# Kernel tuning notes

Hardware: AMD Instinct MI355X
Metric: run time of the kernel (lower is better)

## Reference

```python
import jax, jax.numpy as jnp
import numpy as np

THR = 0.001
EPS = 1e-5
GROUPS = 32

def ternary_weight(w):
    wc = jnp.clip(w, -1.0, 1.0)
    return jnp.where(wc > THR, 1.0, jnp.where(wc < -THR, -1.0, 0.0))

def fake_quant(x, scale):
    s = jnp.abs(scale)
    return jnp.clip(jnp.round(x / s), -1.0, 1.0) * s

def group_norm(x, gamma, beta):
    b, c, h, w = x.shape
    xg = x.reshape(b, GROUPS, c // GROUPS, h, w)
    mu = xg.mean(axis=(2, 3, 4), keepdims=True)
    var = xg.var(axis=(2, 3, 4), keepdims=True)
    xn = (xg - mu) * jax.lax.rsqrt(var + EPS)
    return xn.reshape(b, c, h, w) * gamma[None, :, None, None] + beta[None, :, None, None]

def conv2d(x, w, b, pad):
    out = jax.lax.conv_general_dilated(x, w, (1, 1), [(pad, pad), (pad, pad)],
                                       dimension_numbers=('NCHW', 'OIHW', 'NCHW'))
    return out + b[None, :, None, None]

def setup_inputs() -> dict:
    key = jax.random.key(0)
    ks = jax.random.split(key, 10)
    B, Cin, Cout, H, W, T = 8, 256, 256, 64, 64, 512
    return {
        'x': jax.random.normal(ks[0], (B, Cin, H, W), jnp.float32),
        'time_emb': jax.random.normal(ks[1], (B, T), jnp.float32),
        'gn1_g': jnp.ones((Cin,), jnp.float32),
        'gn1_b': jnp.zeros((Cin,), jnp.float32),
        'scale1': jnp.array(1.0, jnp.float32),
        'W1': jax.random.normal(ks[2], (Cout, Cin, 3, 3), jnp.float32) * 0.05,
        'b1': jax.random.normal(ks[3], (Cout,), jnp.float32) * 0.01,
        'Wt': jax.random.normal(ks[4], (Cout, T), jnp.float32) * 0.05,
        'bt': jax.random.normal(ks[5], (Cout,), jnp.float32) * 0.01,
        'gn2_g': jnp.ones((Cout,), jnp.float32),
        'gn2_b': jnp.zeros((Cout,), jnp.float32),
        'scale2': jnp.array(1.0, jnp.float32),
        'W2': jax.random.normal(ks[6], (Cout, Cout, 3, 3), jnp.float32) * 0.05,
        'b2': jax.random.normal(ks[7], (Cout,), jnp.float32) * 0.01,
    }

def reference(x, time_emb, gn1_g, gn1_b, scale1, W1, b1, Wt, bt, gn2_g, gn2_b, scale2, W2, b2):
    out = group_norm(x, gn1_g, gn1_b)
    out = jax.nn.relu(out)
    out = fake_quant(out, scale1)
    out = conv2d(out, ternary_weight(W1), b1, pad=1)
    # time conditioning: ternary linear on relu(time_emb), broadcast over HW
    tb = jax.nn.relu(time_emb) @ ternary_weight(Wt).T + bt
    out = out + tb[:, :, None, None]
    out = group_norm(out, gn2_g, gn2_b)
    out = jax.nn.relu(out)
    out = fake_quant(out, scale2)
    out = conv2d(out, ternary_weight(W2), b2, pad=1)
    # dropout p=0 (eval) and identity residual (in_channels == out_channels)
    return out + x
```

## Files before the change

kernel.cpp:

```cpp
#include <hip/hip_runtime.h>

typedef float f32x4 __attribute__((ext_vector_type(4)));
typedef __bf16 bf16x8 __attribute__((ext_vector_type(8)));
typedef unsigned int u32;

#define WTHR 0.001f

static constexpr size_t WS_A1   = 0;
static constexpr size_t WS_A2   = 16777216;
static constexpr size_t WS_OUT1 = 33554432;
static constexpr size_t WS_TW   = 67108864;
static constexpr size_t WS_TB   = 69468160;
static constexpr size_t WS_GN1  = 69476352;
static constexpr size_t WS_GN2  = 69478400;

__global__ __launch_bounds__(256)
void k_gn_stats(const float* __restrict__ x, float* __restrict__ mean, float* __restrict__ rstd)
{
    int bg = blockIdx.x;
    int t = threadIdx.x;
    int lane = t & 63, wv = t >> 6;
    const float4* A = reinterpret_cast<const float4*>(x + (size_t)bg * 32768 + (size_t)t * 128);
    __shared__ float red[4];
    __shared__ float Mv;

    float r0, r1, r2, r3, r4, r5, r6, r7;
    {
        float4 v0 = A[0], v1 = A[1];
        r0 = v0.x; r1 = v0.y; r2 = v0.z; r3 = v0.w;
        r4 = v1.x; r5 = v1.y; r6 = v1.z; r7 = v1.w;
        for (int i = 2; i < 32; i += 2) {
            float4 u0 = A[i], u1 = A[i + 1];
            r0 += u0.x; r1 += u0.y; r2 += u0.z; r3 += u0.w;
            r4 += u1.x; r5 += u1.y; r6 += u1.z; r7 += u1.w;
        }
    }
    float p = ((r0 + r1) + (r2 + r3)) + ((r4 + r5) + (r6 + r7));
    #pragma unroll
    for (int st = 1; st <= 32; st <<= 1) p = p + __shfl_down(p, st);
    if (lane == 0) red[wv] = p;
    __syncthreads();
    if (t == 0) Mv = ((red[0] + red[1]) + (red[2] + red[3])) / 32768.0f;
    __syncthreads();
    float mn = Mv;

    {
        float4 v0 = A[0], v1 = A[1];
        float d;
        d = v0.x - mn; r0 = __fmul_rn(d, d);
        d = v0.y - mn; r1 = __fmul_rn(d, d);
        d = v0.z - mn; r2 = __fmul_rn(d, d);
        d = v0.w - mn; r3 = __fmul_rn(d, d);
        d = v1.x - mn; r4 = __fmul_rn(d, d);
        d = v1.y - mn; r5 = __fmul_rn(d, d);
        d = v1.z - mn; r6 = __fmul_rn(d, d);
        d = v1.w - mn; r7 = __fmul_rn(d, d);
        for (int i = 2; i < 32; i += 2) {
            float4 u0 = A[i], u1 = A[i + 1];
            d = u0.x - mn; r0 = r0 + __fmul_rn(d, d);
            d = u0.y - mn; r1 = r1 + __fmul_rn(d, d);
            d = u0.z - mn; r2 = r2 + __fmul_rn(d, d);
            d = u0.w - mn; r3 = r3 + __fmul_rn(d, d);
            d = u1.x - mn; r4 = r4 + __fmul_rn(d, d);
            d = u1.y - mn; r5 = r5 + __fmul_rn(d, d);
            d = u1.z - mn; r6 = r6 + __fmul_rn(d, d);
            d = u1.w - mn; r7 = r7 + __fmul_rn(d, d);
        }
    }
    p = ((r0 + r1) + (r2 + r3)) + ((r4 + r5) + (r6 + r7));
    #pragma unroll
    for (int st = 1; st <= 32; st <<= 1) p = p + __shfl_down(p, st);
    if (lane == 0) red[wv] = p;
    __syncthreads();
    if (t == 0) {
        float var = ((red[0] + red[1]) + (red[2] + red[3])) / 32768.0f;
        mean[bg] = mn;
        rstd[bg] = __fdiv_rn(1.0f, __fsqrt_rn(var + 1e-5f));
    }
}

__global__ __launch_bounds__(256)
void k_tern(const float* __restrict__ W1, const float* __restrict__ W2, unsigned short* __restrict__ twT)
{
    int idx = blockIdx.x * 256 + threadIdx.x;
    int sel = idx >= 589824;
    const float* W = sel ? W2 : W1;
    int lid = idx - (sel ? 589824 : 0);
    int off = lid >> 16;
    int rem = lid & 65535;
    int co = rem >> 8, ci = rem & 255;
    float w = W[(size_t)((co << 8) | ci) * 9 + off];
    unsigned short tq = (w > WTHR) ? (unsigned short)0x3F80u
                      : ((w < -WTHR) ? (unsigned short)0xBF80u : (unsigned short)0u);
    twT[idx] = tq;
}

__global__ __launch_bounds__(256)
void k_tb(const float* __restrict__ te, const float* __restrict__ Wt, const float* __restrict__ bt,
          float* __restrict__ tb)
{
    int b = blockIdx.x, co = threadIdx.x;
    const float* wrow = Wt + (size_t)co * 512;
    const float* trow = te + (size_t)b * 512;
    float acc = 0.f;
    for (int t = 0; t < 512; ++t) {
        float w = wrow[t];
        float tw = (w > WTHR) ? 1.f : ((w < -WTHR) ? -1.f : 0.f);
        acc = __fmaf_rn(fmaxf(trow[t], 0.f), tw, acc);
    }
    tb[(b << 8) + co] = acc + bt[co];
}

__global__ __launch_bounds__(256)
void k_norm_quant(const float* __restrict__ x, const float* __restrict__ gamma, const float* __restrict__ beta,
                  const float* __restrict__ mean, const float* __restrict__ rstd,
                  const float* __restrict__ scale, unsigned short* __restrict__ a)
{
    int blk = blockIdx.x;
    int b = blk >> 6, h = blk & 63;
    int tid = threadIdx.x;
    __shared__ unsigned short T[64 * 264];
    float s = fabsf(*scale);
    int w = tid & 63;
    int c0 = (tid >> 6) << 6;
    for (int o = 0; o < 8; ++o) {
        alignas(16) unsigned short r8[8];
        int bg = (b << 5) + ((c0 >> 3) + o);
        float mnv = mean[bg], rsv = rstd[bg];
        #pragma unroll
        for (int j = 0; j < 8; ++j) {
            int c = c0 + (o << 3) + j;
            float xv = x[((size_t)((b << 8) + c) << 12) + (h << 6) + w];
            float y = __fmul_rn(xv - mnv, rsv);
            y = y * gamma[c] + beta[c];
            y = fmaxf(y, 0.f);
            r8[j] = (rintf(__fdiv_rn(y, s)) >= 1.0f) ? (unsigned short)0x3F80u : (unsigned short)0u;
        }
        *reinterpret_cast<uint4*>(&T[w * 264 + c0 + (o << 3)]) = *reinterpret_cast<const uint4*>(r8);
    }
    __syncthreads();
    unsigned short* dst = a + ((size_t)blk << 14);
    #pragma unroll
    for (int j = 0; j < 8; ++j) {
        int e = (j << 11) + (tid << 3);
        int ww = e >> 8, c = e & 255;
        *reinterpret_cast<uint4*>(dst + e) = *reinterpret_cast<const uint4*>(&T[ww * 264 + c]);
    }
}

template<int O>
__global__ __launch_bounds__(256, 4)
void k_conv(const unsigned short* __restrict__ acts,
            const unsigned short* __restrict__ twT,
            const float* __restrict__ bias,
            const float* __restrict__ tb,
            const float* __restrict__ scale,
            const float* __restrict__ resid,
            float* __restrict__ out)
{
    int blk0 = blockIdx.x;
    int logical = ((blk0 & 7) << 7) + (blk0 >> 3);
    int half = logical & 1;
    int bh = logical >> 1;
    int b = bh >> 6, h = bh & 63;
    int tid = threadIdx.x;
    int lane = tid & 63, wv = tid >> 6;
    int l15 = lane & 15, l4 = lane >> 4;

    __shared__ unsigned short Ls[3 * 64 * 64];

    f32x4 acc[2][4];
    #pragma unroll
    for (int i = 0; i < 2; ++i)
        #pragma unroll
        for (int j = 0; j < 4; ++j) acc[i][j] = (f32x4){0.f, 0.f, 0.f, 0.f};

    int lw = lane >> 3;
    int lc = (lane & 7) ^ lw;
    int cobase = (half << 7) + (wv << 5);

    for (int cc = 0; cc < 4; ++cc) {
        __syncthreads();
        #pragma unroll
        for (int i = 0; i < 6; ++i) {
            int chunk = wv * 6 + i;
            int dh = chunk >> 3;
            int w0 = (chunk & 7) << 3;
            int hh = h + dh - 1;
            char* ldst = (char*)Ls + chunk * 1024;
            if ((unsigned)hh < 64u) {
                const unsigned short* g = acts
                    + ((size_t)(((b << 6) + hh) << 6) + (w0 + lw)) * 256 + (cc << 6) + (lc << 3);
                __builtin_amdgcn_global_load_lds(
                    (const __attribute__((address_space(1))) u32*)g,
                    (__attribute__((address_space(3))) u32*)ldst, 16, 0, 0);
            } else {
                *reinterpret_cast<uint4*>(ldst + lane * 16) = (uint4){0u, 0u, 0u, 0u};
            }
        }
        __syncthreads();

        #pragma unroll
        for (int off = 0; off < 9; ++off) {
            const int kh = off / 3;
            const int kw = off % 3 - 1;
            #pragma unroll
            for (int kk = 0; kk < 2; ++kk) {
                bf16x8 af[4], wf[2];
                #pragma unroll
                for (int nt = 0; nt < 4; ++nt) {
                    int wi = (nt << 4) + l15 + kw;
                    bool ok = (unsigned)wi < 64u;
                    int wc = ok ? wi : 0;
                    int byte = ((kh << 6) + wc) * 128 + (((kk << 6) + (l4 << 4)) ^ ((wc & 7) << 4));
                    uint4 uv = *reinterpret_cast<const uint4*>((const char*)Ls + byte);
                    u32 m = ok ? 0xFFFFFFFFu : 0u;
                    uv.x &= m; uv.y &= m; uv.z &= m; uv.w &= m;
                    af[nt] = *reinterpret_cast<const bf16x8*>(&uv);
                }
                const unsigned short* wb = twT + ((size_t)off << 16)
                    + ((size_t)(cobase + l15) << 8) + (cc << 6) + (kk << 5) + (l4 << 3);
                wf[0] = *reinterpret_cast<const bf16x8*>(wb);
                wf[1] = *reinterpret_cast<const bf16x8*>(wb + 4096);
                #pragma unroll
                for (int mt = 0; mt < 2; ++mt)
                    #pragma unroll
                    for (int nt = 0; nt < 4; ++nt)
                        acc[mt][nt] = __builtin_amdgcn_mfma_f32_16x16x32_bf16(wf[mt], af[nt], acc[mt][nt], 0, 0, 0);
            }
        }
    }

    float qs = fabsf(*scale);
    #pragma unroll
    for (int mt = 0; mt < 2; ++mt)
        #pragma unroll
        for (int r = 0; r < 4; ++r) {
            int co = cobase + (mt << 4) + (l4 << 2) + r;
            float bb = bias[co];
            float tv = (O == 0) ? tb[(b << 8) + co] : 0.f;
            size_t rowb = ((size_t)((b << 8) + co) << 12) + (h << 6);
            #pragma unroll
            for (int nt = 0; nt < 4; ++nt) {
                int w = (nt << 4) + l15;
                float v = __fmul_rn(acc[mt][nt][r], qs) + bb;
                if (O == 0) v = v + tv;
                else        v = v + resid[rowb + w];
                out[rowb + w] = v;
            }
        }
}

extern "C" void kernel_launch(void* const* d_in, const int* in_sizes, int n_in,
                              void* d_out, int out_size, void* d_ws, size_t ws_size,
                              hipStream_t stream)
{
    const float* x      = (const float*)d_in[0];
    const float* te     = (const float*)d_in[1];
    const float* gn1_g  = (const float*)d_in[2];
    const float* gn1_b  = (const float*)d_in[3];
    const float* scale1 = (const float*)d_in[4];
    const float* W1     = (const float*)d_in[5];
    const float* b1     = (const float*)d_in[6];
    const float* Wt     = (const float*)d_in[7];
    const float* bt     = (const float*)d_in[8];
    const float* gn2_g  = (const float*)d_in[9];
    const float* gn2_b  = (const float*)d_in[10];
    const float* scale2 = (const float*)d_in[11];
    const float* W2     = (const float*)d_in[12];
    const float* b2     = (const float*)d_in[13];
    float* out = (float*)d_out;

    char* ws = (char*)d_ws;
    unsigned short* a1   = (unsigned short*)(ws + WS_A1);
    unsigned short* a2   = (unsigned short*)(ws + WS_A2);
    float*          out1 = (float*)(ws + WS_OUT1);
    unsigned short* tw   = (unsigned short*)(ws + WS_TW);
    unsigned short* tw1  = tw;
    unsigned short* tw2  = tw + 589824;
    float*          tbp  = (float*)(ws + WS_TB);
    float*          gn1m = (float*)(ws + WS_GN1);
    float*          gn1r = gn1m + 256;
    float*          gn2m = (float*)(ws + WS_GN2);
    float*          gn2r = gn2m + 256;

    k_gn_stats<<<256, 256, 0, stream>>>(x, gn1m, gn1r);
    k_tern<<<4608, 256, 0, stream>>>(W1, W2, tw);
    k_tb<<<8, 256, 0, stream>>>(te, Wt, bt, tbp);
    k_norm_quant<<<512, 256, 0, stream>>>(x, gn1_g, gn1_b, gn1m, gn1r, scale1, a1);
    k_conv<0><<<1024, 256, 0, stream>>>(a1, tw1, b1, tbp, scale1, nullptr, out1);
    k_gn_stats<<<256, 256, 0, stream>>>(out1, gn2m, gn2r);
    k_norm_quant<<<512, 256, 0, stream>>>(out1, gn2_g, gn2_b, gn2m, gn2r, scale2, a2);
    k_conv<1><<<1024, 256, 0, stream>>>(a2, tw2, b2, nullptr, scale2, x, out);
}
```

Baseline: 322.7 us.

## Double-buffer conv fragment loads, coalesce ternarize, swizzle norm-quant LDS

Three separate changes. The conv inner loop is flattened into 18 steps and loads the next step's LDS activation fragments and global weight fragments into a second register set while the current step's MFMAs run, so load latency can overlap with compute. The ternarize kernel now reads each output channel's weights contiguously into shared memory and writes the transposed layout from there, replacing strided global gathers. The norm-quant transpose buffer drops its padding and uses an XOR swizzle to avoid bank conflicts; the extra live registers in the conv loop may lower occupancy.

```diff
diff --git a/kernel.cpp b/kernel.cpp
--- a/kernel.cpp
+++ b/kernel.cpp
@@ -82,17 +82,25 @@
 __global__ __launch_bounds__(256)
 void k_tern(const float* __restrict__ W1, const float* __restrict__ W2, unsigned short* __restrict__ twT)
 {
-    int idx = blockIdx.x * 256 + threadIdx.x;
-    int sel = idx >= 589824;
-    const float* W = sel ? W2 : W1;
-    int lid = idx - (sel ? 589824 : 0);
-    int off = lid >> 16;
-    int rem = lid & 65535;
-    int co = rem >> 8, ci = rem & 255;
-    float w = W[(size_t)((co << 8) | ci) * 9 + off];
-    unsigned short tq = (w > WTHR) ? (unsigned short)0x3F80u
-                      : ((w < -WTHR) ? (unsigned short)0xBF80u : (unsigned short)0u);
-    twT[idx] = tq;
+    int blk = blockIdx.x;
+    int co = blk & 255;
+    const float* src = ((blk & 256) ? W2 : W1) + (size_t)co * 2304;
+    unsigned short* base = twT + (size_t)(blk >> 8) * 589824 + (co << 8);
+    int t = threadIdx.x;
+    __shared__ unsigned short Q[2304];
+    #pragma unroll
+    for (int i = 0; i < 9; ++i) {
+        float w = src[t + (i << 8)];
+        Q[t + (i << 8)] = (w > WTHR) ? (unsigned short)0x3F80u
+                        : ((w < -WTHR) ? (unsigned short)0xBF80u : (unsigned short)0u);
+    }
+    __syncthreads();
+    #pragma unroll
+    for (int i = 0; i < 9; ++i) {
+        int idx = t + (i << 8);
+        int off = idx >> 8, ci = idx & 255;
+        base[off * 65536 + ci] = Q[ci * 9 + off];
+    }
 }
 
 __global__ __launch_bounds__(256)
@@ -119,32 +127,35 @@
     int blk = blockIdx.x;
     int b = blk >> 6, h = blk & 63;
     int tid = threadIdx.x;
-    __shared__ unsigned short T[64 * 264];
+    __shared__ unsigned short T[64 * 256];
     float s = fabsf(*scale);
     int w = tid & 63;
-    int c0 = (tid >> 6) << 6;
+    int g0 = (tid >> 6) << 3;
+    #pragma unroll
     for (int o = 0; o < 8; ++o) {
+        int gc = g0 + o;
         alignas(16) unsigned short r8[8];
-        int bg = (b << 5) + ((c0 >> 3) + o);
-        float mnv = mean[bg], rsv = rstd[bg];
+        float mnv = mean[(b << 5) + gc], rsv = rstd[(b << 5) + gc];
         #pragma unroll
         for (int j = 0; j < 8; ++j) {
-            int c = c0 + (o << 3) + j;
+            int c = (gc << 3) + j;
             float xv = x[((size_t)((b << 8) + c) << 12) + (h << 6) + w];
             float y = __fmul_rn(xv - mnv, rsv);
             y = y * gamma[c] + beta[c];
             y = fmaxf(y, 0.f);
             r8[j] = (rintf(__fdiv_rn(y, s)) >= 1.0f) ? (unsigned short)0x3F80u : (unsigned short)0u;
         }
-        *reinterpret_cast<uint4*>(&T[w * 264 + c0 + (o << 3)]) = *reinterpret_cast<const uint4*>(r8);
+        int gs = gc ^ (w & 31);
+        *reinterpret_cast<uint4*>(&T[(w << 8) + (gs << 3)]) = *reinterpret_cast<const uint4*>(r8);
     }
     __syncthreads();
     unsigned short* dst = a + ((size_t)blk << 14);
     #pragma unroll
     for (int j = 0; j < 8; ++j) {
         int e = (j << 11) + (tid << 3);
-        int ww = e >> 8, c = e & 255;
-        *reinterpret_cast<uint4*>(dst + e) = *reinterpret_cast<const uint4*>(&T[ww * 264 + c]);
+        int ww = e >> 8;
+        int gs = (tid & 31) ^ (ww & 31);
+        *reinterpret_cast<uint4*>(dst + e) = *reinterpret_cast<const uint4*>(&T[(ww << 8) + (gs << 3)]);
     }
 }
 
@@ -200,34 +211,43 @@
         }
         __syncthreads();
 
-        #pragma unroll
-        for (int off = 0; off < 9; ++off) {
-            const int kh = off / 3;
-            const int kw = off % 3 - 1;
+        auto loadStep = [&](int s, bf16x8* af, bf16x8* wf) {
+            int off = s >> 1;
+            int kh = off / 3;
+            int kwv = off % 3 - 1;
+            int kk = s & 1;
             #pragma unroll
-            for (int kk = 0; kk < 2; ++kk) {
-                bf16x8 af[4], wf[2];
+            for (int nt = 0; nt < 4; ++nt) {
+                int wi = (nt << 4) + l15 + kwv;
+                bool ok = (unsigned)wi < 64u;
+                int wc = ok ? wi : 0;
+                int byte = ((kh << 6) + wc) * 128 + (((kk << 6) + (l4 << 4)) ^ ((wc & 7) << 4));
+                uint4 uv = *reinterpret_cast<const uint4*>((const char*)Ls + byte);
+                u32 m = ok ? 0xFFFFFFFFu : 0u;
+                uv.x &= m; uv.y &= m; uv.z &= m; uv.w &= m;
+                af[nt] = *reinterpret_cast<const bf16x8*>(&uv);
+            }
+            const unsigned short* wb = twT + ((size_t)off << 16)
+                + ((size_t)(cobase + l15) << 8) + (cc << 6) + (kk << 5) + (l4 << 3);
+            wf[0] = *reinterpret_cast<const bf16x8*>(wb);
+            wf[1] = *reinterpret_cast<const bf16x8*>(wb + 4096);
+        };
+
+        bf16x8 afA[4], afB[4], wfA[2], wfB[2];
+        loadStep(0, afA, wfA);
+        #pragma unroll
+        for (int s = 0; s < 18; ++s) {
+            if (s < 17) {
+                if (s & 1) loadStep(s + 1, afA, wfA);
+                else       loadStep(s + 1, afB, wfB);
+            }
+            const bf16x8* af = (s & 1) ? afB : afA;
+            const bf16x8* wf = (s & 1) ? wfB : wfA;
+            #pragma unroll
+            for (int mt = 0; mt < 2; ++mt)
                 #pragma unroll
-                for (int nt = 0; nt < 4; ++nt) {
-                    int wi = (nt << 4) + l15 + kw;
-                    bool ok = (unsigned)wi < 64u;
-                    int wc = ok ? wi : 0;
-                    int byte = ((kh << 6) + wc) * 128 + (((kk << 6) + (l4 << 4)) ^ ((wc & 7) << 4));
-                    uint4 uv = *reinterpret_cast<const uint4*>((const char*)Ls + byte);
-                    u32 m = ok ? 0xFFFFFFFFu : 0u;
-                    uv.x &= m; uv.y &= m; uv.z &= m; uv.w &= m;
-                    af[nt] = *reinterpret_cast<const bf16x8*>(&uv);
-                }
-                const unsigned short* wb = twT + ((size_t)off << 16)
-                    + ((size_t)(cobase + l15) << 8) + (cc << 6) + (kk << 5) + (l4 << 3);
-                wf[0] = *reinterpret_cast<const bf16x8*>(wb);
-                wf[1] = *reinterpret_cast<const bf16x8*>(wb + 4096);
-                #pragma unroll
-                for (int mt = 0; mt < 2; ++mt)
-                    #pragma unroll
-                    for (int nt = 0; nt < 4; ++nt)
-                        acc[mt][nt] = __builtin_amdgcn_mfma_f32_16x16x32_bf16(wf[mt], af[nt], acc[mt][nt], 0, 0, 0);
-            }
+                for (int nt = 0; nt < 4; ++nt)
+                    acc[mt][nt] = __builtin_amdgcn_mfma_f32_16x16x32_bf16(wf[mt], af[nt], acc[mt][nt], 0, 0, 0);
         }
     }
 
@@ -285,7 +305,7 @@
     float*          gn2r = gn2m + 256;
 
     k_gn_stats<<<256, 256, 0, stream>>>(x, gn1m, gn1r);
-    k_tern<<<4608, 256, 0, stream>>>(W1, W2, tw);
+    k_tern<<<512, 256, 0, stream>>>(W1, W2, tw);
     k_tb<<<8, 256, 0, stream>>>(te, Wt, bt, tbp);
     k_norm_quant<<<512, 256, 0, stream>>>(x, gn1_g, gn1_b, gn1m, gn1r, scale1, a1);
     k_conv<0><<<1024, 256, 0, stream>>>(a1, tw1, b1, tbp, scale1, nullptr, out1);
```

Result: no change. 318.7 us (-1.2%).
